# Kernel optimization log

Measured on AMD Instinct MI355X. Metric: run time of the kernel, lower is better.

The kernel has to match this reference:

```python
import jax, jax.numpy as jnp
import numpy as np

EMB_DIM = 1024
NUM_HEADS = 16
SCALE_WEIGHTS = 1.0
TINY = jnp.finfo(jnp.float32).tiny


def setup_inputs() -> dict:
    key = jax.random.key(0)
    k1, k2, k3 = jax.random.split(key, 3)
    B, S = 2, 2048
    x = jax.random.normal(k1, (B, S, EMB_DIM), dtype=jnp.float32)
    weights = jax.random.uniform(k2, (B, S), dtype=jnp.float32)
    W_qkv = jax.random.normal(k3, (EMB_DIM, 3 * EMB_DIM), dtype=jnp.float32) / np.sqrt(EMB_DIM)
    b_qkv = jnp.zeros((3 * EMB_DIM,), dtype=jnp.float32)
    return {"x": x, "weights": weights, "W_qkv": W_qkv, "b_qkv": b_qkv}


def reference(x, weights, W_qkv, b_qkv):
    B, S, E = x.shape
    H = NUM_HEADS
    hd = E // H
    # QKV projection: [B,S,3E] -> [B,H,S,3*hd] -> split
    qkv = x @ W_qkv + b_qkv
    qkv = qkv.reshape(B, S, H, 3 * hd).transpose(0, 2, 1, 3)
    q, k, v = jnp.split(qkv, 3, axis=-1)  # each [B,H,S,hd]
    # weights: [B,S] -> [B,1,1,S] (broadcast over heads and query positions)
    w = weights[:, None, None, :]
    # scores with log-weight bias and hard masks
    attn_logits = jnp.einsum("bhqd,bhkd->bhqk", q, k) / jnp.sqrt(jnp.asarray(hd, x.dtype))
    attn_logits = attn_logits + jnp.log(w / SCALE_WEIGHTS + TINY)
    attn_logits = jnp.where(w == 0, -9e15, attn_logits)
    attn_logits = jnp.where(w == 1, 9e15, attn_logits)
    attention = jax.nn.softmax(attn_logits, axis=-1)
    values = jnp.einsum("bhqk,bhkd->bhqd", attention, v)
    return values.transpose(0, 2, 1, 3).reshape(B, S, E)
```

## Files before the change

### kernel.cpp

```cpp
#include <hip/hip_runtime.h>
#include <math.h>

#define B_  2
#define S_  2048
#define E_  1024
#define H_  16
#define HD_ 64
#define N3_ 3072
#define M_  (B_*S_)
#define NROWS_ (32 * S_)

typedef _Float16 h8  __attribute__((ext_vector_type(8)));
typedef _Float16 h4  __attribute__((ext_vector_type(4)));
typedef __fp16   fp16v2 __attribute__((ext_vector_type(2)));
typedef float    f4  __attribute__((ext_vector_type(4)));
typedef float    fv16 __attribute__((ext_vector_type(16)));

typedef __attribute__((address_space(3))) unsigned int       lds_u32;
typedef const __attribute__((address_space(1))) unsigned int glob_u32;

__device__ __forceinline__ void gld16(const void* g, void* l) {
    __builtin_amdgcn_global_load_lds((glob_u32*)g, (lds_u32*)l, 16, 0, 0);
}
__device__ __forceinline__ float exp2_hw(float x) { return __builtin_amdgcn_exp2f(x); }
__device__ __forceinline__ h4 pack4(float a, float b, float c, float d) {
    union { struct { fp16v2 l, h; } p; h4 v; } u;
    u.p.l = __builtin_amdgcn_cvt_pkrtz(a, b);
    u.p.h = __builtin_amdgcn_cvt_pkrtz(c, d);
    return u.v;
}

#define QSCALE 0.18033688011112042f
#define FMAX_  8.0f

__global__ void cvt_x_kernel(const float* __restrict__ x, _Float16* __restrict__ x16) {
    int i = (blockIdx.x * 256 + threadIdx.x) * 8;
    float4 u = *(const float4*)&x[i];
    float4 v = *(const float4*)&x[i + 4];
    h8 o;
    o[0] = (_Float16)u.x; o[1] = (_Float16)u.y; o[2] = (_Float16)u.z; o[3] = (_Float16)u.w;
    o[4] = (_Float16)v.x; o[5] = (_Float16)v.y; o[6] = (_Float16)v.z; o[7] = (_Float16)v.w;
    *(h8*)&x16[i] = o;
}

__global__ __launch_bounds__(256) void transpose_w_kernel(
        const float* __restrict__ W, _Float16* __restrict__ Wt) {
    __shared__ float T[64][65];
    int k0 = blockIdx.x * 64, n0 = blockIdx.y * 64;
    int tid = threadIdx.x;
    int r = tid >> 4, c4 = (tid & 15) * 4;
#pragma unroll
    for (int i = 0; i < 4; i++) {
        int row = r + i * 16;
        float4 u = *(const float4*)&W[(size_t)(k0 + row) * N3_ + n0 + c4];
        T[c4 + 0][row] = u.x; T[c4 + 1][row] = u.y;
        T[c4 + 2][row] = u.z; T[c4 + 3][row] = u.w;
    }
    __syncthreads();
#pragma unroll
    for (int i = 0; i < 4; i++) {
        int rn = r + i * 16;
        h4 p;
        p[0] = (_Float16)T[rn][c4 + 0]; p[1] = (_Float16)T[rn][c4 + 1];
        p[2] = (_Float16)T[rn][c4 + 2]; p[3] = (_Float16)T[rn][c4 + 3];
        *(h4*)&Wt[(size_t)(n0 + rn) * E_ + k0 + c4] = p;
    }
}

__global__ __launch_bounds__(256, 2) void qkv_gemm32(
        const _Float16* __restrict__ x16, const _Float16* __restrict__ wt,
        const float* __restrict__ bq, const float* __restrict__ w,
        _Float16* __restrict__ qws, _Float16* __restrict__ kws,
        _Float16* __restrict__ vtws) {
    __shared__ __align__(16) _Float16 Ab[2][128 * 64];
    __shared__ __align__(16) _Float16 Wb[2][192 * 64];

    int tid = threadIdx.x;
    int wid = tid >> 6, lane = tid & 63;
    int l31 = lane & 31, hi = lane >> 5, l7 = l31 & 7;
    int srow = lane >> 3;
    int wm = wid & 1, wn = wid >> 1;

    int L = blockIdx.x;
    int head = 2 * (L & 7) + (L >> 8);
    int mb = (L >> 3) & 31;
    int m0 = mb * 128;
    int n0 = head * 192;
    int b = m0 >> 11;
    int bh = b * H_ + head;
    int sblk = m0 & 2047;

    fv16 acc[2][3];
#pragma unroll
    for (int ntl = 0; ntl < 3; ntl++) {
        int n_abs = wn * 96 + ntl * 32;
        int which = n_abs >> 6;
        fv16 ini;
        if (which == 2) {
            float bb = bq[n0 + n_abs + l31];
#pragma unroll
            for (int r = 0; r < 16; r++) ini[r] = bb;
        } else {
#pragma unroll
            for (int g = 0; g < 4; g++) {
                f4 bv = *(const f4*)&bq[n0 + n_abs + 8 * g + 4 * hi];
#pragma unroll
                for (int j = 0; j < 4; j++) ini[4 * g + j] = bv[j];
            }
        }
        acc[0][ntl] = ini; acc[1][ntl] = ini;
    }

    auto stage = [&](int t, int bf) {
        int k0 = t * 64;
#pragma unroll
        for (int j = 0; j < 4; j++) {
            int batch = wid * 4 + j;
            int row = batch * 8 + srow;
            int ch = (lane & 7) ^ srow ^ (batch & 7);
            gld16(&x16[(size_t)(m0 + row) * E_ + k0 + ch * 8], &Ab[bf][batch * 8 * 64]);
        }
#pragma unroll
        for (int j = 0; j < 6; j++) {
            int batch = wid * 6 + j;
            int row = batch * 8 + srow;
            int ch = (lane & 7) ^ srow ^ (batch & 7);
            gld16(&wt[(size_t)(n0 + row) * E_ + k0 + ch * 8], &Wb[bf][batch * 8 * 64]);
        }
    };

    stage(0, 0);

    for (int t = 0; t < 16; t++) {
        int bf = t & 1;
        __syncthreads();
        if (t < 15) stage(t + 1, bf ^ 1);
#pragma unroll
        for (int step = 0; step < 4; step++) {
            h8 af[2], wf[3];
#pragma unroll
            for (int mt = 0; mt < 2; mt++) {
                int R = wm * 64 + mt * 32 + l31;
                int ph = ((2 * step + hi) ^ l7 ^ ((mt * 4 + (l31 >> 3)) & 7)) * 8;
                af[mt] = *(const h8*)&Ab[bf][R * 64 + ph];
            }
#pragma unroll
            for (int ntl = 0; ntl < 3; ntl++) {
                int R = wn * 96 + ntl * 32 + l31;
                int ph = ((2 * step + hi) ^ l7 ^ ((wn * 12 + ntl * 4 + (l31 >> 3)) & 7)) * 8;
                wf[ntl] = *(const h8*)&Wb[bf][R * 64 + ph];
            }
#pragma unroll
            for (int ntl = 0; ntl < 3; ntl++) {
                bool isv = (wn == 1) && (ntl >= 1);
#pragma unroll
                for (int mt = 0; mt < 2; mt++) {
                    if (isv)
                        acc[mt][ntl] = __builtin_amdgcn_mfma_f32_32x32x16_f16(af[mt], wf[ntl], acc[mt][ntl], 0, 0, 0);
                    else
                        acc[mt][ntl] = __builtin_amdgcn_mfma_f32_32x32x16_f16(wf[ntl], af[mt], acc[mt][ntl], 0, 0, 0);
                }
            }
        }
    }

#pragma unroll
    for (int ntl = 0; ntl < 3; ntl++) {
        int n_abs = wn * 96 + ntl * 32;
        int which = n_abs >> 6;
#pragma unroll
        for (int mt = 0; mt < 2; mt++) {
            if (which == 2) {
                int d = (n_abs & 63) + l31;
#pragma unroll
                for (int g = 0; g < 4; g++) {
                    int soff = wm * 64 + mt * 32 + 8 * g + 4 * hi;
                    f4 wf4 = *(const f4*)&w[m0 + soff];
                    h4 p = pack4(acc[mt][ntl][4 * g + 0] * wf4[0],
                                 acc[mt][ntl][4 * g + 1] * wf4[1],
                                 acc[mt][ntl][4 * g + 2] * wf4[2],
                                 acc[mt][ntl][4 * g + 3] * wf4[3]);
                    *(h4*)&vtws[((size_t)bh * 64 + d) * S_ + sblk + soff] = p;
                }
            } else {
                _Float16* dst = (which == 0) ? qws : kws;
                float scale = (which == 0) ? QSCALE : 1.0f;
                int s = sblk + wm * 64 + mt * 32 + l31;
#pragma unroll
                for (int g = 0; g < 4; g++) {
                    int d0 = (n_abs & 63) + 8 * g + 4 * hi;
                    h4 p = pack4(acc[mt][ntl][4 * g + 0] * scale,
                                 acc[mt][ntl][4 * g + 1] * scale,
                                 acc[mt][ntl][4 * g + 2] * scale,
                                 acc[mt][ntl][4 * g + 3] * scale);
                    *(h4*)&dst[((size_t)bh * S_ + s) * 64 + d0] = p;
                }
            }
        }
    }
}

__global__ __launch_bounds__(256, 4) void attn_kernel(
        const _Float16* __restrict__ q, const _Float16* __restrict__ k,
        const _Float16* __restrict__ vt, const float* __restrict__ w,
        _Float16* __restrict__ opart, float* __restrict__ ml) {
    __shared__ __align__(16) _Float16 Kb[2][64 * 64];
    __shared__ __align__(16) _Float16 Vb[2][64 * 64];
    __shared__ __align__(16) float lws[1024];

    int tid = threadIdx.x;
    int wid = tid >> 6, lane = tid & 63;
    int l31 = lane & 31, hi = lane >> 5, l7 = l31 & 7;
    int srow = lane >> 3;
    int L = blockIdx.x;
    int bh = (L & 7) + 8 * (L >> 8);
    int qt = (L >> 3) & 15;
    int half = (L >> 7) & 1;
    int q0 = qt * 128;
    int kh0 = half * 1024;
    int b = bh >> 4;

    const _Float16* qbase = q + (size_t)bh * S_ * HD_;
    const _Float16* kbase = k + (size_t)bh * S_ * HD_;
    const _Float16* vbase = vt + (size_t)bh * HD_ * S_;
    const float* wbase = w + (size_t)b * S_;

    gld16(&wbase[kh0 + wid * 256 + lane * 4], &lws[wid * 256]);

    auto stage = [&](int kt, int bf) {
        int k0 = kh0 + kt * 64;
#pragma unroll
        for (int j = 0; j < 2; j++) {
            int batch = wid * 2 + j;
            int row = batch * 8 + srow;
            int ch = (lane & 7) ^ srow ^ (batch & 7);
            gld16(&kbase[(size_t)(k0 + row) * 64 + ch * 8], &Kb[bf][batch * 8 * 64]);
            gld16(&vbase[(size_t)row * S_ + k0 + ch * 8], &Vb[bf][batch * 8 * 64]);
        }
    };

    stage(0, 0);

    int qrow = q0 + wid * 32 + l31;
    h8 qf[4];
#pragma unroll
    for (int step = 0; step < 4; step++)
        qf[step] = *(const h8*)&qbase[(size_t)qrow * 64 + 16 * step + 8 * hi];

    fv16 o[2];
    o[0] = (fv16)0.0f; o[1] = (fv16)0.0f;
    float l_r = 0.0f;

    for (int kt = 0; kt < 16; kt++) {
        int bf = kt & 1;
        __syncthreads();
        if (kt < 15) stage(kt + 1, bf ^ 1);

        fv16 st[2];
        st[0] = (fv16)0.0f; st[1] = (fv16)0.0f;
#pragma unroll
        for (int step = 0; step < 4; step++) {
#pragma unroll
            for (int kt2 = 0; kt2 < 2; kt2++) {
                int R = kt2 * 32 + l31;
                int ph = ((2 * step + hi) ^ l7 ^ ((kt2 * 4 + (l31 >> 3)) & 7)) * 8;
                h8 kf = *(const h8*)&Kb[bf][R * 64 + ph];
                st[kt2] = __builtin_amdgcn_mfma_f32_32x32x16_f16(kf, qf[step], st[kt2], 0, 0, 0);
            }
        }

        h4 pf[2][4];
        int kk = kt * 64;
#pragma unroll
        for (int kt2 = 0; kt2 < 2; kt2++)
#pragma unroll
            for (int g = 0; g < 4; g++) {
                f4 wv = *(const f4*)&lws[kk + kt2 * 32 + 8 * g + 4 * hi];
                float e0 = exp2_hw(st[kt2][4 * g + 0] - FMAX_);
                float e1 = exp2_hw(st[kt2][4 * g + 1] - FMAX_);
                float e2 = exp2_hw(st[kt2][4 * g + 2] - FMAX_);
                float e3 = exp2_hw(st[kt2][4 * g + 3] - FMAX_);
                l_r = fmaf(e0, wv[0], l_r); l_r = fmaf(e1, wv[1], l_r);
                l_r = fmaf(e2, wv[2], l_r); l_r = fmaf(e3, wv[3], l_r);
                pf[kt2][g] = pack4(e0, e1, e2, e3);
            }

#pragma unroll
        for (int kt2 = 0; kt2 < 2; kt2++)
#pragma unroll
            for (int g = 0; g < 4; g++) {
                int c = 4 * kt2 + g;
#pragma unroll
                for (int dt = 0; dt < 2; dt++) {
                    int R = dt * 32 + l31;
                    int ph = (c ^ l7 ^ ((dt * 4 + (l31 >> 3)) & 7)) * 8 + hi * 4;
                    h4 vf = *(const h4*)&Vb[bf][R * 64 + ph];
                    o[dt] = __builtin_amdgcn_mfma_f32_32x32x8f16(vf, pf[kt2][g], o[dt], 0, 0, 0);
                }
            }
    }

    l_r += __shfl_xor(l_r, 32);
    size_t prow = (size_t)(half * 32 + bh) * S_ + qrow;
    float linv = 1.0f / l_r;
    _Float16* obase = &opart[prow * 64];
#pragma unroll
    for (int dt = 0; dt < 2; dt++)
#pragma unroll
        for (int g = 0; g < 4; g++) {
            int d0 = dt * 32 + 8 * g + 4 * hi;
            h4 p = pack4(o[dt][4 * g + 0] * linv, o[dt][4 * g + 1] * linv,
                         o[dt][4 * g + 2] * linv, o[dt][4 * g + 3] * linv);
            *(h4*)&obase[d0] = p;
        }
    if (hi == 0) ml[prow] = l_r;
}

__global__ __launch_bounds__(256) void combine_kernel(
        const _Float16* __restrict__ opart, const float* __restrict__ ml,
        float* __restrict__ out) {
    int t = threadIdx.x;
    int r = blockIdx.x * 16 + (t >> 4);
    int dg = (t & 15) * 4;
    int bh = r >> 11, qrow = r & 2047;
    float l0 = ml[r];
    float l1 = ml[NROWS_ + r];
    float inv = 1.0f / (l0 + l1);
    float w0 = l0 * inv, w1 = l1 * inv;
    h4 a = *(const h4*)&opart[(size_t)r * 64 + dg];
    h4 c = *(const h4*)&opart[((size_t)NROWS_ + r) * 64 + dg];
    f4 o;
#pragma unroll
    for (int j = 0; j < 4; j++) o[j] = (float)a[j] * w0 + (float)c[j] * w1;
    *(f4*)&out[((size_t)((bh >> 4) * S_ + qrow)) * E_ + (bh & 15) * 64 + dg] = o;
}

extern "C" void kernel_launch(void* const* d_in, const int* in_sizes, int n_in,
                              void* d_out, int out_size, void* d_ws, size_t ws_size,
                              hipStream_t stream) {
    const float* x  = (const float*)d_in[0];
    const float* w  = (const float*)d_in[1];
    const float* Wq = (const float*)d_in[2];
    const float* bq = (const float*)d_in[3];
    float* out = (float*)d_out;

    char* p = (char*)d_ws;
    _Float16* x16 = (_Float16*)p;              p += (size_t)M_ * E_ * 2;
    _Float16* wt  = (_Float16*)p;              p += (size_t)E_ * N3_ * 2;
    _Float16* qb  = (_Float16*)p;              p += (size_t)M_ * E_ * 2;
    _Float16* kb  = (_Float16*)p;              p += (size_t)M_ * E_ * 2;
    _Float16* vtb = (_Float16*)p;              p += (size_t)M_ * E_ * 2;
    _Float16* opart = (_Float16*)p;            p += (size_t)2 * NROWS_ * 64 * 2;
    float* mlb = (float*)p;

    cvt_x_kernel<<<dim3(M_ * E_ / 2048), dim3(256), 0, stream>>>(x, x16);
    transpose_w_kernel<<<dim3(E_ / 64, N3_ / 64), dim3(256), 0, stream>>>(Wq, wt);
    qkv_gemm32<<<dim3(512), dim3(256), 0, stream>>>(x16, wt, bq, w, qb, kb, vtb);
    attn_kernel<<<dim3(1024), dim3(256), 0, stream>>>(qb, kb, vtb, w, opart, mlb);
    combine_kernel<<<dim3(NROWS_ / 16), dim3(256), 0, stream>>>(opart, mlb, out);
}
```

Measured before the change: 182.6 us.

## Merge prep kernels, shrink QKV GEMM N-tile to 64, fold max offset into score init

The fp32-to-fp16 conversion of x and the transpose of W are merged into one launch, removing a kernel launch. The QKV GEMM drops from 128x192 tiles (512 blocks) to 128x64 tiles (1536 blocks) with less LDS and occupancy raised to 3 blocks per CU. This improves parallelism but reloads each x tile three times as often. In attention, the constant max subtraction moves into the score accumulator's initial value, and the row sum is split into two accumulators to shorten the dependency chain.

```diff
diff --git a/kernel.cpp b/kernel.cpp
--- a/kernel.cpp
+++ b/kernel.cpp
@@ -33,21 +33,24 @@
 #define QSCALE 0.18033688011112042f
 #define FMAX_  8.0f
 
-__global__ void cvt_x_kernel(const float* __restrict__ x, _Float16* __restrict__ x16) {
-    int i = (blockIdx.x * 256 + threadIdx.x) * 8;
-    float4 u = *(const float4*)&x[i];
-    float4 v = *(const float4*)&x[i + 4];
-    h8 o;
-    o[0] = (_Float16)u.x; o[1] = (_Float16)u.y; o[2] = (_Float16)u.z; o[3] = (_Float16)u.w;
-    o[4] = (_Float16)v.x; o[5] = (_Float16)v.y; o[6] = (_Float16)v.z; o[7] = (_Float16)v.w;
-    *(h8*)&x16[i] = o;
-}
-
-__global__ __launch_bounds__(256) void transpose_w_kernel(
+__global__ __launch_bounds__(256) void prep_kernel(
+        const float* __restrict__ x, _Float16* __restrict__ x16,
         const float* __restrict__ W, _Float16* __restrict__ Wt) {
     __shared__ float T[64][65];
-    int k0 = blockIdx.x * 64, n0 = blockIdx.y * 64;
+    int blk = blockIdx.x;
     int tid = threadIdx.x;
+    if (blk < 2048) {
+        int i = (blk * 256 + tid) * 8;
+        float4 u = *(const float4*)&x[i];
+        float4 v = *(const float4*)&x[i + 4];
+        h8 o;
+        o[0] = (_Float16)u.x; o[1] = (_Float16)u.y; o[2] = (_Float16)u.z; o[3] = (_Float16)u.w;
+        o[4] = (_Float16)v.x; o[5] = (_Float16)v.y; o[6] = (_Float16)v.z; o[7] = (_Float16)v.w;
+        *(h8*)&x16[i] = o;
+        return;
+    }
+    int idx = blk - 2048;
+    int k0 = (idx & 15) * 64, n0 = (idx >> 4) * 64;
     int r = tid >> 4, c4 = (tid & 15) * 4;
 #pragma unroll
     for (int i = 0; i < 4; i++) {
@@ -67,13 +70,13 @@
     }
 }
 
-__global__ __launch_bounds__(256, 2) void qkv_gemm32(
+__global__ __launch_bounds__(256, 3) void qkv_gemm32(
         const _Float16* __restrict__ x16, const _Float16* __restrict__ wt,
         const float* __restrict__ bq, const float* __restrict__ w,
         _Float16* __restrict__ qws, _Float16* __restrict__ kws,
         _Float16* __restrict__ vtws) {
     __shared__ __align__(16) _Float16 Ab[2][128 * 64];
-    __shared__ __align__(16) _Float16 Wb[2][192 * 64];
+    __shared__ __align__(16) _Float16 Wb[2][64 * 64];
 
     int tid = threadIdx.x;
     int wid = tid >> 6, lane = tid & 63;
@@ -82,33 +85,32 @@
     int wm = wid & 1, wn = wid >> 1;
 
     int L = blockIdx.x;
-    int head = 2 * (L & 7) + (L >> 8);
-    int mb = (L >> 3) & 31;
+    int mb = L / 48, nt = L % 48;
     int m0 = mb * 128;
-    int n0 = head * 192;
+    int n0 = nt * 64;
+    int head = n0 / 192;
+    int which = (n0 % 192) / 64;
+    bool isV = (which == 2);
     int b = m0 >> 11;
     int bh = b * H_ + head;
     int sblk = m0 & 2047;
 
-    fv16 acc[2][3];
-#pragma unroll
-    for (int ntl = 0; ntl < 3; ntl++) {
-        int n_abs = wn * 96 + ntl * 32;
-        int which = n_abs >> 6;
+    fv16 acc[2];
+    if (isV) {
+        float bb = bq[n0 + wn * 32 + l31];
         fv16 ini;
-        if (which == 2) {
-            float bb = bq[n0 + n_abs + l31];
-#pragma unroll
-            for (int r = 0; r < 16; r++) ini[r] = bb;
-        } else {
-#pragma unroll
-            for (int g = 0; g < 4; g++) {
-                f4 bv = *(const f4*)&bq[n0 + n_abs + 8 * g + 4 * hi];
-#pragma unroll
-                for (int j = 0; j < 4; j++) ini[4 * g + j] = bv[j];
-            }
-        }
-        acc[0][ntl] = ini; acc[1][ntl] = ini;
+#pragma unroll
+        for (int r = 0; r < 16; r++) ini[r] = bb;
+        acc[0] = ini; acc[1] = ini;
+    } else {
+        fv16 ini;
+#pragma unroll
+        for (int g = 0; g < 4; g++) {
+            f4 bv = *(const f4*)&bq[n0 + wn * 32 + 8 * g + 4 * hi];
+#pragma unroll
+            for (int j = 0; j < 4; j++) ini[4 * g + j] = bv[j];
+        }
+        acc[0] = ini; acc[1] = ini;
     }
 
     auto stage = [&](int t, int bf) {
@@ -121,8 +123,8 @@
             gld16(&x16[(size_t)(m0 + row) * E_ + k0 + ch * 8], &Ab[bf][batch * 8 * 64]);
         }
 #pragma unroll
-        for (int j = 0; j < 6; j++) {
-            int batch = wid * 6 + j;
+        for (int j = 0; j < 2; j++) {
+            int batch = wid * 2 + j;
             int row = batch * 8 + srow;
             int ch = (lane & 7) ^ srow ^ (batch & 7);
             gld16(&wt[(size_t)(n0 + row) * E_ + k0 + ch * 8], &Wb[bf][batch * 8 * 64]);
@@ -137,64 +139,58 @@
         if (t < 15) stage(t + 1, bf ^ 1);
 #pragma unroll
         for (int step = 0; step < 4; step++) {
-            h8 af[2], wf[3];
+            h8 af[2], wf;
 #pragma unroll
             for (int mt = 0; mt < 2; mt++) {
                 int R = wm * 64 + mt * 32 + l31;
                 int ph = ((2 * step + hi) ^ l7 ^ ((mt * 4 + (l31 >> 3)) & 7)) * 8;
                 af[mt] = *(const h8*)&Ab[bf][R * 64 + ph];
             }
-#pragma unroll
-            for (int ntl = 0; ntl < 3; ntl++) {
-                int R = wn * 96 + ntl * 32 + l31;
-                int ph = ((2 * step + hi) ^ l7 ^ ((wn * 12 + ntl * 4 + (l31 >> 3)) & 7)) * 8;
-                wf[ntl] = *(const h8*)&Wb[bf][R * 64 + ph];
-            }
-#pragma unroll
-            for (int ntl = 0; ntl < 3; ntl++) {
-                bool isv = (wn == 1) && (ntl >= 1);
-#pragma unroll
-                for (int mt = 0; mt < 2; mt++) {
-                    if (isv)
-                        acc[mt][ntl] = __builtin_amdgcn_mfma_f32_32x32x16_f16(af[mt], wf[ntl], acc[mt][ntl], 0, 0, 0);
-                    else
-                        acc[mt][ntl] = __builtin_amdgcn_mfma_f32_32x32x16_f16(wf[ntl], af[mt], acc[mt][ntl], 0, 0, 0);
-                }
-            }
-        }
-    }
-
-#pragma unroll
-    for (int ntl = 0; ntl < 3; ntl++) {
-        int n_abs = wn * 96 + ntl * 32;
-        int which = n_abs >> 6;
+            {
+                int R = wn * 32 + l31;
+                int ph = ((2 * step + hi) ^ l7 ^ ((wn * 4 + (l31 >> 3)) & 7)) * 8;
+                wf = *(const h8*)&Wb[bf][R * 64 + ph];
+            }
+            if (isV) {
+#pragma unroll
+                for (int mt = 0; mt < 2; mt++)
+                    acc[mt] = __builtin_amdgcn_mfma_f32_32x32x16_f16(af[mt], wf, acc[mt], 0, 0, 0);
+            } else {
+#pragma unroll
+                for (int mt = 0; mt < 2; mt++)
+                    acc[mt] = __builtin_amdgcn_mfma_f32_32x32x16_f16(wf, af[mt], acc[mt], 0, 0, 0);
+            }
+        }
+    }
+
+    if (isV) {
+        int d = wn * 32 + l31;
+#pragma unroll
+        for (int mt = 0; mt < 2; mt++)
+#pragma unroll
+            for (int g = 0; g < 4; g++) {
+                int soff = wm * 64 + mt * 32 + 8 * g + 4 * hi;
+                f4 wf4 = *(const f4*)&w[m0 + soff];
+                h4 p = pack4(acc[mt][4 * g + 0] * wf4[0],
+                             acc[mt][4 * g + 1] * wf4[1],
+                             acc[mt][4 * g + 2] * wf4[2],
+                             acc[mt][4 * g + 3] * wf4[3]);
+                *(h4*)&vtws[((size_t)bh * 64 + d) * S_ + sblk + soff] = p;
+            }
+    } else {
+        _Float16* dst = (which == 0) ? qws : kws;
+        float scale = (which == 0) ? QSCALE : 1.0f;
 #pragma unroll
         for (int mt = 0; mt < 2; mt++) {
-            if (which == 2) {
-                int d = (n_abs & 63) + l31;
-#pragma unroll
-                for (int g = 0; g < 4; g++) {
-                    int soff = wm * 64 + mt * 32 + 8 * g + 4 * hi;
-                    f4 wf4 = *(const f4*)&w[m0 + soff];
-                    h4 p = pack4(acc[mt][ntl][4 * g + 0] * wf4[0],
-                                 acc[mt][ntl][4 * g + 1] * wf4[1],
-                                 acc[mt][ntl][4 * g + 2] * wf4[2],
-                                 acc[mt][ntl][4 * g + 3] * wf4[3]);
-                    *(h4*)&vtws[((size_t)bh * 64 + d) * S_ + sblk + soff] = p;
-                }
-            } else {
-                _Float16* dst = (which == 0) ? qws : kws;
-                float scale = (which == 0) ? QSCALE : 1.0f;
-                int s = sblk + wm * 64 + mt * 32 + l31;
-#pragma unroll
-                for (int g = 0; g < 4; g++) {
-                    int d0 = (n_abs & 63) + 8 * g + 4 * hi;
-                    h4 p = pack4(acc[mt][ntl][4 * g + 0] * scale,
-                                 acc[mt][ntl][4 * g + 1] * scale,
-                                 acc[mt][ntl][4 * g + 2] * scale,
-                                 acc[mt][ntl][4 * g + 3] * scale);
-                    *(h4*)&dst[((size_t)bh * S_ + s) * 64 + d0] = p;
-                }
+            int s = sblk + wm * 64 + mt * 32 + l31;
+#pragma unroll
+            for (int g = 0; g < 4; g++) {
+                int d0 = wn * 32 + 8 * g + 4 * hi;
+                h4 p = pack4(acc[mt][4 * g + 0] * scale,
+                             acc[mt][4 * g + 1] * scale,
+                             acc[mt][4 * g + 2] * scale,
+                             acc[mt][4 * g + 3] * scale);
+                *(h4*)&dst[((size_t)bh * S_ + s) * 64 + d0] = p;
             }
         }
     }
@@ -249,7 +245,7 @@
 
     fv16 o[2];
     o[0] = (fv16)0.0f; o[1] = (fv16)0.0f;
-    float l_r = 0.0f;
+    float l0a = 0.0f, l1a = 0.0f;
 
     for (int kt = 0; kt < 16; kt++) {
         int bf = kt & 1;
@@ -257,7 +253,7 @@
         if (kt < 15) stage(kt + 1, bf ^ 1);
 
         fv16 st[2];
-        st[0] = (fv16)0.0f; st[1] = (fv16)0.0f;
+        st[0] = (fv16)(-FMAX_); st[1] = (fv16)(-FMAX_);
 #pragma unroll
         for (int step = 0; step < 4; step++) {
 #pragma unroll
@@ -276,12 +272,17 @@
 #pragma unroll
             for (int g = 0; g < 4; g++) {
                 f4 wv = *(const f4*)&lws[kk + kt2 * 32 + 8 * g + 4 * hi];
-                float e0 = exp2_hw(st[kt2][4 * g + 0] - FMAX_);
-                float e1 = exp2_hw(st[kt2][4 * g + 1] - FMAX_);
-                float e2 = exp2_hw(st[kt2][4 * g + 2] - FMAX_);
-                float e3 = exp2_hw(st[kt2][4 * g + 3] - FMAX_);
-                l_r = fmaf(e0, wv[0], l_r); l_r = fmaf(e1, wv[1], l_r);
-                l_r = fmaf(e2, wv[2], l_r); l_r = fmaf(e3, wv[3], l_r);
+                float e0 = exp2_hw(st[kt2][4 * g + 0]);
+                float e1 = exp2_hw(st[kt2][4 * g + 1]);
+                float e2 = exp2_hw(st[kt2][4 * g + 2]);
+                float e3 = exp2_hw(st[kt2][4 * g + 3]);
+                if (kt2 == 0) {
+                    l0a = fmaf(e0, wv[0], l0a); l0a = fmaf(e1, wv[1], l0a);
+                    l0a = fmaf(e2, wv[2], l0a); l0a = fmaf(e3, wv[3], l0a);
+                } else {
+                    l1a = fmaf(e0, wv[0], l1a); l1a = fmaf(e1, wv[1], l1a);
+                    l1a = fmaf(e2, wv[2], l1a); l1a = fmaf(e3, wv[3], l1a);
+                }
                 pf[kt2][g] = pack4(e0, e1, e2, e3);
             }
 
@@ -300,6 +301,7 @@
             }
     }
 
+    float l_r = l0a + l1a;
     l_r += __shfl_xor(l_r, 32);
     size_t prow = (size_t)(half * 32 + bh) * S_ + qrow;
     float linv = 1.0f / l_r;
@@ -353,9 +355,8 @@
     _Float16* opart = (_Float16*)p;            p += (size_t)2 * NROWS_ * 64 * 2;
     float* mlb = (float*)p;
 
-    cvt_x_kernel<<<dim3(M_ * E_ / 2048), dim3(256), 0, stream>>>(x, x16);
-    transpose_w_kernel<<<dim3(E_ / 64, N3_ / 64), dim3(256), 0, stream>>>(Wq, wt);
-    qkv_gemm32<<<dim3(512), dim3(256), 0, stream>>>(x16, wt, bq, w, qb, kb, vtb);
+    prep_kernel<<<dim3(2048 + 768), dim3(256), 0, stream>>>(x, x16, Wq, wt);
+    qkv_gemm32<<<dim3(1536), dim3(256), 0, stream>>>(x16, wt, bq, w, qb, kb, vtb);
     attn_kernel<<<dim3(1024), dim3(256), 0, stream>>>(qb, kb, vtb, w, opart, mlb);
     combine_kernel<<<dim3(NROWS_ / 16), dim3(256), 0, stream>>>(opart, mlb, out);
 }
```

After: 294.2 us. 61.1% more time.
